# Kernel optimization log

Measured on AMD Instinct MI355X. Metric: run time of the kernel, lower is better.

## Reference

```python
import jax, jax.numpy as jnp
import numpy as np

N = 100000   # num_nodes
E = 1600000  # num_edges
H = 128      # hidden_dim
OUT = 1      # output_dim
SLOPE = 0.2  # GATConv leaky_relu negative_slope


def setup_inputs() -> dict:
    key = jax.random.key(0)
    ks = jax.random.split(key, 10)
    s = 1.0 / np.sqrt(H)
    return {
        "h": jnp.arange(N, dtype=jnp.int64 if jax.config.jax_enable_x64 else jnp.int32),
        "edge_index": jax.random.randint(ks[0], (2, E), 0, N),
        "node_type": jax.random.randint(ks[1], (N,), 0, 3),
        "emb": jax.random.normal(ks[2], (N, H), jnp.float32) * s,
        "W1": jax.random.normal(ks[3], (H, H), jnp.float32) * s,
        "a_src1": jax.random.normal(ks[4], (H,), jnp.float32) * s,
        "a_dst1": jax.random.normal(ks[5], (H,), jnp.float32) * s,
        "b1": jnp.zeros((H,), jnp.float32),
        "W2": jax.random.normal(ks[6], (H, OUT), jnp.float32) * s,
        "a_src2": jax.random.normal(ks[7], (OUT,), jnp.float32) * s,
        "a_dst2": jax.random.normal(ks[8], (OUT,), jnp.float32) * s,
        "b2": jnp.zeros((OUT,), jnp.float32),
    }


def gat_layer(x, src, dst, emask, W, a_src, a_dst, b, n_nodes):
    """PyG GATConv (heads=1, add_self_loops=True). Masked edges get -inf logits."""
    xp = x @ W                                  # [N, F]
    e_src = xp @ a_src                          # [N]
    e_dst = xp @ a_dst                          # [N]
    logits = jax.nn.leaky_relu(e_src[src] + e_dst[dst], SLOPE)   # [E]
    logits = jnp.where(emask, logits, -jnp.inf)
    self_logits = jax.nn.leaky_relu(e_src + e_dst, SLOPE)        # [N] self-loops
    # segment softmax over destination nodes (edges + self loop)
    m = jax.ops.segment_max(logits, dst, num_segments=n_nodes)
    m = jnp.maximum(m, self_logits)             # finite: self loop always present
    ew = jnp.exp(logits - m[dst])               # masked edges -> exp(-inf)=0
    sw = jnp.exp(self_logits - m)
    denom = jax.ops.segment_sum(ew, dst, num_segments=n_nodes) + sw
    alpha = ew / denom[dst]                     # [E]
    alpha_self = sw / denom                     # [N]
    out = jax.ops.segment_sum(alpha[:, None] * xp[src], dst, num_segments=n_nodes)
    out = out + alpha_self[:, None] * xp + b
    return out


def reference(h, edge_index, node_type, emb, W1, a_src1, a_dst1, b1, W2, a_src2, a_dst2, b2):
    src, dst = edge_index[0], edge_index[1]
    emask = (node_type[src] == 0) & (node_type[dst] == 0)
    x = emb[h]                                          # embedding lookup [N, H]
    x = gat_layer(x, src, dst, emask, W1, a_src1, a_dst1, b1, emb.shape[0])
    x = jax.nn.relu(x)
    x = gat_layer(x, src, dst, emask, W2, a_src2, a_dst2, b2, emb.shape[0])
    return x
```

## Files before the change

### kernel.cpp

```cpp
#include <hip/hip_runtime.h>

#define N_NODES 100000
#define N_EDGES 1600000
#define HD 128
#define SLOPE 0.2f
#define NBLK 391
#define GB 782
#define EB3 1563
#define CAP 32
#define SLICE_LD 136
#define K2B 2048

typedef __attribute__((ext_vector_type(8))) short bf16x8;
typedef __attribute__((ext_vector_type(4))) float f32x4;

__device__ __forceinline__ unsigned short f2bf(float f) {
    union { float f; unsigned u; } v; v.f = f;
    const unsigned u = v.u + 0x7FFFu + ((v.u >> 16) & 1u);
    return (unsigned short)(u >> 16);
}
__device__ __forceinline__ unsigned pack2(float lo, float hi) {
    return (unsigned)f2bf(lo) | ((unsigned)f2bf(hi) << 16);
}
__device__ __forceinline__ float bf2f(unsigned u16) {
    union { unsigned u; float f; } v; v.u = u16 << 16; return v.f;
}

__global__ __launch_bounds__(256) void k0_zero(
    const int* __restrict__ nt, const float* __restrict__ W1,
    int* __restrict__ deg, unsigned* __restrict__ umask,
    unsigned short* __restrict__ W1bfT)
{
    const int i = blockIdx.x * 256 + threadIdx.x;
    bool act = false;
    if (i < N_NODES) { deg[i] = 0; act = (nt[i] == 0); }
    const unsigned long long bal = __ballot(act);
    const int lane = threadIdx.x & 63;
    if (lane == 0)       umask[i >> 5] = (unsigned)bal;
    else if (lane == 32) umask[i >> 5] = (unsigned)(bal >> 32);
    if (i < HD * HD) {
        const int n = i >> 7, k = i & 127;
        W1bfT[n * HD + k] = f2bf(W1[k * HD + n]);
    }
}

__global__ __launch_bounds__(512) void k1a_edge(
    const int* __restrict__ ei, const unsigned* __restrict__ umask,
    int* __restrict__ deg, int* __restrict__ adj)
{
    const int t = blockIdx.x * 512 + threadIdx.x;
    const int e0 = t * 2;
    if (e0 >= N_EDGES) return;
    const int2 s2 = *(const int2*)(ei + e0);
    const int2 d2 = *(const int2*)(ei + N_EDGES + e0);
    const bool a0 =
        (((umask[s2.x >> 5] >> (s2.x & 31)) & (umask[d2.x >> 5] >> (d2.x & 31))) & 1u) != 0u;
    const bool a1 =
        (((umask[s2.y >> 5] >> (s2.y & 31)) & (umask[d2.y >> 5] >> (d2.y & 31))) & 1u) != 0u;
    if (a0) {
        const int sl = atomicAdd(deg + d2.x, 1);
        if (sl < CAP) adj[(size_t)d2.x * CAP + sl] = s2.x;
    }
    if (a1) {
        const int sl = atomicAdd(deg + d2.y, 1);
        if (sl < CAP) adj[(size_t)d2.y * CAP + sl] = s2.y;
    }
}

__global__ __launch_bounds__(512, 8) void k1b_gemm(
    const int* __restrict__ h,
    const float* __restrict__ emb,
    const unsigned short* __restrict__ W1bfT,
    const float* __restrict__ a_src1,
    const float* __restrict__ a_dst1,
    unsigned short* __restrict__ xp1,
    float* __restrict__ es1,
    float* __restrict__ ed1,
    float* __restrict__ denom1)
{
    __shared__ unsigned short Wlds[8 * 16 * SLICE_LD];
    const int tid = threadIdx.x;

    {
        const int n  = tid >> 2;
        const int kq = (tid & 3) * 32;
        const unsigned short* src = W1bfT + n * HD + kq;
        #pragma unroll
        for (int j = 0; j < 4; ++j) {
            const int c = (kq >> 3) + j;
            const int p = c ^ (n & 7);
            *(bf16x8*)(Wlds + n * HD + p * 8) = *(const bf16x8*)(src + j * 8);
        }
    }

    const int w   = tid >> 6;
    const int L   = tid & 63;
    const int lm  = L & 15;
    const int lg  = L >> 4;
    const int wrow0 = blockIdx.x * 128 + w * 16;

    const int arow = wrow0 + lm;
    const int g = (arow < N_NODES) ? arow : (N_NODES - 1);
    const float* xrow = emb + (size_t)h[g] * HD;

    __syncthreads();

    f32x4 acc[8];
    #pragma unroll
    for (int ct = 0; ct < 8; ++ct) acc[ct] = (f32x4)0.f;

    #pragma unroll
    for (int ks = 0; ks < 4; ++ks) {
        const int k0 = ks * 32 + lg * 8;
        const float4 u = *(const float4*)(xrow + k0);
        const float4 v = *(const float4*)(xrow + k0 + 4);
        union { bf16x8 b; unsigned x[4]; } t;
        t.x[0] = pack2(u.x, u.y);
        t.x[1] = pack2(u.z, u.w);
        t.x[2] = pack2(v.x, v.y);
        t.x[3] = pack2(v.z, v.w);
        const bf16x8 af = t.b;

        const int c = k0 >> 3;
        const int p = (c ^ (lm & 7)) * 8;
        #pragma unroll
        for (int ct = 0; ct < 8; ++ct) {
            const bf16x8 bfr = *(const bf16x8*)(Wlds + (ct * 16 + lm) * HD + p);
            acc[ct] = __builtin_amdgcn_mfma_f32_16x16x32_bf16(af, bfr, acc[ct], 0, 0, 0);
        }
    }

    float asv[8], adv[8];
    #pragma unroll
    for (int ct = 0; ct < 8; ++ct) {
        asv[ct] = a_src1[ct * 16 + lm];
        adv[ct] = a_dst1[ct * 16 + lm];
    }

    #pragma unroll
    for (int reg = 0; reg < 4; ++reg) {
        const int row = wrow0 + lg * 4 + reg;
        float s = 0.f, d = 0.f;
        #pragma unroll
        for (int ct = 0; ct < 8; ++ct) {
            s += acc[ct][reg] * asv[ct];
            d += acc[ct][reg] * adv[ct];
        }
        #pragma unroll
        for (int m = 1; m < 16; m <<= 1) {
            s += __shfl_xor(s, m, 64);
            d += __shfl_xor(d, m, 64);
        }
        if (row < N_NODES && lm == 0) {
            const float sum = s + d;
            const float l = sum > 0.f ? sum : SLOPE * sum;
            es1[row] = s;
            ed1[row] = d;
            denom1[row] = __expf(l);
        }
    }

    __syncthreads();
    unsigned short* slice = Wlds + w * 16 * SLICE_LD;
    #pragma unroll
    for (int ct = 0; ct < 8; ++ct)
        #pragma unroll
        for (int reg = 0; reg < 4; ++reg)
            slice[(lg * 4 + reg) * SLICE_LD + ct * 16 + lm] = f2bf(acc[ct][reg]);
    __syncthreads();
    #pragma unroll
    for (int rr = 0; rr < 4; ++rr) {
        const int rl = rr * 4 + lg;
        const int row = wrow0 + rl;
        if (row < N_NODES) {
            const bf16x8 vdat = *(const bf16x8*)(slice + rl * SLICE_LD + lm * 8);
            *(bf16x8*)(xp1 + (size_t)row * HD + lm * 8) = vdat;
        }
    }
}

__global__ __launch_bounds__(256) void k2_gather(
    const unsigned short* __restrict__ xp1, const float* __restrict__ denom1,
    const float* __restrict__ es1, const float* __restrict__ ed1,
    const int* __restrict__ deg, const int* __restrict__ adj,
    const float* __restrict__ b1, const float* __restrict__ W2,
    float* __restrict__ xp2)
{
    const int wid = threadIdx.x >> 6;
    const int lane = threadIdx.x & 63;
    const float b1a = b1[2 * lane], b1b = b1[2 * lane + 1];
    const float w2a = W2[2 * lane], w2b = W2[2 * lane + 1];

    for (int i = blockIdx.x * 4 + wid; i < N_NODES; i += K2B * 4) {
        const int dcount = min(deg[i], CAP);

        const unsigned pself = ((const unsigned*)(xp1 + (size_t)i * HD))[lane];
        float a0 = bf2f(pself & 0xFFFFu);
        float a1 = bf2f(pself >> 16);

        if (dcount > 0) {
            const float wself = denom1[i];
            const float edv   = ed1[i];
            const int* arow = adj + (size_t)i * CAP;

            int nidx = 0; float nw = 0.f;
            if (lane < dcount) {
                nidx = arow[lane];
                const float lgt = es1[nidx] + edv;
                nw = __expf(lgt > 0.f ? lgt : SLOPE * lgt);
            }
            float dsum = nw;
            #pragma unroll
            for (int m = 32; m > 0; m >>= 1) dsum += __shfl_xor(dsum, m, 64);
            const float inv = 1.f / (wself + dsum);

            a0 *= wself;
            a1 *= wself;

            int j = 0;
            for (; j + 2 <= dcount; j += 2) {
                const int   s0 = __shfl(nidx, j, 64);
                const int   s1 = __shfl(nidx, j + 1, 64);
                const float w0 = __shfl(nw, j, 64);
                const float w1 = __shfl(nw, j + 1, 64);
                const unsigned p0 = ((const unsigned*)(xp1 + (size_t)s0 * HD))[lane];
                const unsigned p1 = ((const unsigned*)(xp1 + (size_t)s1 * HD))[lane];
                a0 += w0 * bf2f(p0 & 0xFFFFu) + w1 * bf2f(p1 & 0xFFFFu);
                a1 += w0 * bf2f(p0 >> 16)     + w1 * bf2f(p1 >> 16);
            }
            if (j < dcount) {
                const int   s0 = __shfl(nidx, j, 64);
                const float w0 = __shfl(nw, j, 64);
                const unsigned p0 = ((const unsigned*)(xp1 + (size_t)s0 * HD))[lane];
                a0 += w0 * bf2f(p0 & 0xFFFFu);
                a1 += w0 * bf2f(p0 >> 16);
            }
            a0 *= inv;
            a1 *= inv;
        }

        const float o0 = fmaxf(a0 + b1a, 0.f);
        const float o1 = fmaxf(a1 + b1b, 0.f);

        float part = o0 * w2a + o1 * w2b;
        #pragma unroll
        for (int off = 32; off > 0; off >>= 1) part += __shfl_down(part, off, 64);
        if (lane == 0) xp2[i] = part;
    }
}

__global__ __launch_bounds__(256) void k3_final(
    const float* __restrict__ xp2, const int* __restrict__ deg,
    const int* __restrict__ adj,
    const float* __restrict__ a_src2, const float* __restrict__ a_dst2,
    const float* __restrict__ b2, float* __restrict__ out)
{
    const int i = blockIdx.x * 256 + threadIdx.x;
    if (i >= N_NODES) return;

    const float xi = xp2[i];
    const int dcount = min(deg[i], CAP);
    if (dcount == 0) {
        out[i] = xi + b2[0];
        return;
    }

    const float as = a_src2[0], ad = a_dst2[0];
    const float adxi = ad * xi;
    const float s0 = (as + ad) * xi;
    const float l0 = s0 > 0.f ? s0 : SLOPE * s0;
    const float wself = __expf(l0);

    float denom = wself, num = wself * xi;
    const int* arow = adj + (size_t)i * CAP;

    int j = 0;
    for (; j + 2 <= dcount; j += 2) {
        const int2 ss = *(const int2*)(arow + j);
        const float x0 = xp2[ss.x];
        const float x1 = xp2[ss.y];
        float l0e = as * x0 + adxi; l0e = l0e > 0.f ? l0e : SLOPE * l0e;
        float l1e = as * x1 + adxi; l1e = l1e > 0.f ? l1e : SLOPE * l1e;
        const float w0 = __expf(l0e);
        const float w1 = __expf(l1e);
        denom += w0 + w1;
        num   += w0 * x0 + w1 * x1;
    }
    if (j < dcount) {
        const float x0 = xp2[arow[j]];
        float l0e = as * x0 + adxi; l0e = l0e > 0.f ? l0e : SLOPE * l0e;
        const float w0 = __expf(l0e);
        denom += w0;
        num   += w0 * x0;
    }
    out[i] = num / denom + b2[0];
}

extern "C" void kernel_launch(void* const* d_in, const int* in_sizes, int n_in,
                              void* d_out, int out_size, void* d_ws, size_t ws_size,
                              hipStream_t stream)
{
    const int* h   = (const int*)d_in[0];
    const int* ei  = (const int*)d_in[1];
    const int* nt  = (const int*)d_in[2];
    const float* emb    = (const float*)d_in[3];
    const float* W1     = (const float*)d_in[4];
    const float* a_src1 = (const float*)d_in[5];
    const float* a_dst1 = (const float*)d_in[6];
    const float* b1     = (const float*)d_in[7];
    const float* W2     = (const float*)d_in[8];
    const float* a_src2 = (const float*)d_in[9];
    const float* a_dst2 = (const float*)d_in[10];
    const float* b2     = (const float*)d_in[11];
    float* out = (float*)d_out;

    char* ws = (char*)d_ws;
    size_t off = 0;
    unsigned short* xp1 = (unsigned short*)(ws + off); off += (size_t)N_NODES * HD * sizeof(unsigned short);
    float* es1    = (float*)(ws + off); off += (size_t)N_NODES * sizeof(float);
    float* ed1    = (float*)(ws + off); off += (size_t)N_NODES * sizeof(float);
    float* denom1 = (float*)(ws + off); off += (size_t)N_NODES * sizeof(float);
    float* xp2    = (float*)(ws + off); off += (size_t)N_NODES * sizeof(float);
    int*   deg    = (int*)(ws + off);   off += (size_t)N_NODES * sizeof(int);
    unsigned* umask = (unsigned*)(ws + off); off += 3200 * sizeof(unsigned);
    unsigned short* W1bfT = (unsigned short*)(ws + off); off += (size_t)HD * HD * sizeof(unsigned short);
    off = (off + 255) & ~(size_t)255;
    int*   adj    = (int*)(ws + off);   off += (size_t)N_NODES * CAP * sizeof(int);

    k0_zero<<<NBLK, 256, 0, stream>>>(nt, W1, deg, umask, W1bfT);
    k1a_edge<<<EB3, 512, 0, stream>>>(ei, umask, deg, adj);
    k1b_gemm<<<GB, 512, 0, stream>>>(
        h, emb, W1bfT, a_src1, a_dst1, xp1, es1, ed1, denom1);
    k2_gather<<<K2B, 256, 0, stream>>>(
        xp1, denom1, es1, ed1, deg, adj, b1, W2, xp2);
    k3_final<<<NBLK, 256, 0, stream>>>(
        xp2, deg, adj, a_src2, a_dst2, b2, out);
}
```

Measured before the change: 176.3 us.

## Fuse edge-bucketing and GEMM kernels into one launch via block-index split

Merges the edge adjacency-building kernel and the layer-1 GEMM kernel into a single launch in which the first blocks do edge bucketing and the remaining blocks do the GEMM. The two independent workloads can then overlap on the GPU and one launch gap goes away. It also moves the zero-degree output write from the final kernel into the gather kernel, so the final kernel exits early for those nodes. The edge blocks now carry the GEMM kernel's shared memory and launch bounds, which may reduce their occupancy.

```diff
diff --git a/kernel.cpp b/kernel.cpp
--- a/kernel.cpp
+++ b/kernel.cpp
@@ -44,30 +44,11 @@
     }
 }
 
-__global__ __launch_bounds__(512) void k1a_edge(
-    const int* __restrict__ ei, const unsigned* __restrict__ umask,
-    int* __restrict__ deg, int* __restrict__ adj)
-{
-    const int t = blockIdx.x * 512 + threadIdx.x;
-    const int e0 = t * 2;
-    if (e0 >= N_EDGES) return;
-    const int2 s2 = *(const int2*)(ei + e0);
-    const int2 d2 = *(const int2*)(ei + N_EDGES + e0);
-    const bool a0 =
-        (((umask[s2.x >> 5] >> (s2.x & 31)) & (umask[d2.x >> 5] >> (d2.x & 31))) & 1u) != 0u;
-    const bool a1 =
-        (((umask[s2.y >> 5] >> (s2.y & 31)) & (umask[d2.y >> 5] >> (d2.y & 31))) & 1u) != 0u;
-    if (a0) {
-        const int sl = atomicAdd(deg + d2.x, 1);
-        if (sl < CAP) adj[(size_t)d2.x * CAP + sl] = s2.x;
-    }
-    if (a1) {
-        const int sl = atomicAdd(deg + d2.y, 1);
-        if (sl < CAP) adj[(size_t)d2.y * CAP + sl] = s2.y;
-    }
-}
-
-__global__ __launch_bounds__(512, 8) void k1b_gemm(
+__global__ __launch_bounds__(512, 8) void k1_fused(
+    const int* __restrict__ ei,
+    const unsigned* __restrict__ umask,
+    int* __restrict__ deg,
+    int* __restrict__ adj,
     const int* __restrict__ h,
     const float* __restrict__ emb,
     const unsigned short* __restrict__ W1bfT,
@@ -81,6 +62,28 @@
     __shared__ unsigned short Wlds[8 * 16 * SLICE_LD];
     const int tid = threadIdx.x;
 
+    if (blockIdx.x < EB3) {
+        const int t = blockIdx.x * 512 + tid;
+        const int e0 = t * 2;
+        if (e0 >= N_EDGES) return;
+        const int2 s2 = *(const int2*)(ei + e0);
+        const int2 d2 = *(const int2*)(ei + N_EDGES + e0);
+        const bool a0 =
+            (((umask[s2.x >> 5] >> (s2.x & 31)) & (umask[d2.x >> 5] >> (d2.x & 31))) & 1u) != 0u;
+        const bool a1 =
+            (((umask[s2.y >> 5] >> (s2.y & 31)) & (umask[d2.y >> 5] >> (d2.y & 31))) & 1u) != 0u;
+        if (a0) {
+            const int sl = atomicAdd(deg + d2.x, 1);
+            if (sl < CAP) adj[(size_t)d2.x * CAP + sl] = s2.x;
+        }
+        if (a1) {
+            const int sl = atomicAdd(deg + d2.y, 1);
+            if (sl < CAP) adj[(size_t)d2.y * CAP + sl] = s2.y;
+        }
+        return;
+    }
+    const int vb = blockIdx.x - EB3;
+
     {
         const int n  = tid >> 2;
         const int kq = (tid & 3) * 32;
@@ -97,7 +100,7 @@
     const int L   = tid & 63;
     const int lm  = L & 15;
     const int lg  = L >> 4;
-    const int wrow0 = blockIdx.x * 128 + w * 16;
+    const int wrow0 = vb * 128 + w * 16;
 
     const int arow = wrow0 + lm;
     const int g = (arow < N_NODES) ? arow : (N_NODES - 1);
@@ -184,12 +187,14 @@
     const float* __restrict__ es1, const float* __restrict__ ed1,
     const int* __restrict__ deg, const int* __restrict__ adj,
     const float* __restrict__ b1, const float* __restrict__ W2,
-    float* __restrict__ xp2)
+    const float* __restrict__ b2,
+    float* __restrict__ xp2, float* __restrict__ out)
 {
     const int wid = threadIdx.x >> 6;
     const int lane = threadIdx.x & 63;
     const float b1a = b1[2 * lane], b1b = b1[2 * lane + 1];
     const float w2a = W2[2 * lane], w2b = W2[2 * lane + 1];
+    const float b2v = b2[0];
 
     for (int i = blockIdx.x * 4 + wid; i < N_NODES; i += K2B * 4) {
         const int dcount = min(deg[i], CAP);
@@ -245,7 +250,10 @@
         float part = o0 * w2a + o1 * w2b;
         #pragma unroll
         for (int off = 32; off > 0; off >>= 1) part += __shfl_down(part, off, 64);
-        if (lane == 0) xp2[i] = part;
+        if (lane == 0) {
+            xp2[i] = part;
+            if (dcount == 0) out[i] = part + b2v;
+        }
     }
 }
 
@@ -258,13 +266,10 @@
     const int i = blockIdx.x * 256 + threadIdx.x;
     if (i >= N_NODES) return;
 
+    const int dcount = min(deg[i], CAP);
+    if (dcount == 0) return;
+
     const float xi = xp2[i];
-    const int dcount = min(deg[i], CAP);
-    if (dcount == 0) {
-        out[i] = xi + b2[0];
-        return;
-    }
-
     const float as = a_src2[0], ad = a_dst2[0];
     const float adxi = ad * xi;
     const float s0 = (as + ad) * xi;
@@ -328,11 +333,11 @@
     int*   adj    = (int*)(ws + off);   off += (size_t)N_NODES * CAP * sizeof(int);
 
     k0_zero<<<NBLK, 256, 0, stream>>>(nt, W1, deg, umask, W1bfT);
-    k1a_edge<<<EB3, 512, 0, stream>>>(ei, umask, deg, adj);
-    k1b_gemm<<<GB, 512, 0, stream>>>(
+    k1_fused<<<EB3 + GB, 512, 0, stream>>>(
+        ei, umask, deg, adj,
         h, emb, W1bfT, a_src1, a_dst1, xp1, es1, ed1, denom1);
     k2_gather<<<K2B, 256, 0, stream>>>(
-        xp1, denom1, es1, ed1, deg, adj, b1, W2, xp2);
+        xp1, denom1, es1, ed1, deg, adj, b1, W2, b2, xp2, out);
     k3_final<<<NBLK, 256, 0, stream>>>(
         xp2, deg, adj, a_src2, a_dst2, b2, out);
 }
```

After: 173.3 us. Within noise of the previous version (-1.7%).
